# Kernel tuning notes

Measured on AMD Instinct MI355X. Metric: run time of the kernel, lower is better.

The kernel has to match this reference:

```python
import jax, jax.numpy as jnp
import numpy as np

N = 100_000          # nodes
E = 3_200_000        # edges (avg degree 32)
IN, HID, OUT = 128, 64, 40
POWERS = [6, 8, 10]
MAXP = 10
LN_EPS = 1e-5


def setup_inputs() -> dict:
    key = jax.random.key(0)
    ks = jax.random.split(key, 8)
    x = jax.random.normal(ks[0], (N, IN), jnp.float32)
    edge_index = jax.random.randint(ks[1], (2, E), 0, N, dtype=jnp.int32)
    # params (torch Linear: y = x @ W + b with W stored [in, out] here)
    W1 = jax.random.normal(ks[2], (IN, HID), jnp.float32) / np.sqrt(IN)
    b1 = jnp.zeros((HID,), jnp.float32)
    # MixHopConv has Linear for every power 0..max(powers); only p in POWERS are used
    Wc = jax.random.normal(ks[3], (MAXP + 1, HID, HID), jnp.float32) / np.sqrt(HID)
    bc = jnp.zeros((MAXP + 1, HID), jnp.float32)
    W2 = jax.random.normal(ks[4], (HID * len(POWERS), OUT), jnp.float32) / np.sqrt(HID * len(POWERS))
    b2 = jnp.zeros((OUT,), jnp.float32)
    g1 = jnp.ones((HID,), jnp.float32); be1 = jnp.zeros((HID,), jnp.float32)
    g2 = jnp.ones((HID * len(POWERS),), jnp.float32); be2 = jnp.zeros((HID * len(POWERS),), jnp.float32)
    return dict(x=x, edge_index=edge_index, W1=W1, b1=b1, Wc=Wc, bc=bc,
                W2=W2, b2=b2, g1=g1, be1=be1, g2=g2, be2=be2)


def _layer_norm(h, g, b):
    mu = jnp.mean(h, axis=-1, keepdims=True)
    var = jnp.mean(jnp.square(h - mu), axis=-1, keepdims=True)
    return (h - mu) * jax.lax.rsqrt(var + LN_EPS) * g + b


def _gcn_norm(edge_index, n, dtype):
    # add self loops (fill 1), symmetric normalization D^-1/2 (A+I) D^-1/2
    loops = jnp.arange(n, dtype=edge_index.dtype)
    src = jnp.concatenate([edge_index[0], loops])
    dst = jnp.concatenate([edge_index[1], loops])
    w = jnp.ones(src.shape[0], dtype)
    deg = jax.ops.segment_sum(w, dst, num_segments=n)
    dis = jnp.where(deg > 0, jax.lax.rsqrt(deg), 0.0)
    norm = dis[src] * w * dis[dst]
    return src, dst, norm


def reference(x, edge_index, W1, b1, Wc, bc, W2, b2, g1, be1, g2, be2):
    n = x.shape[0]
    src, dst, norm = _gcn_norm(edge_index, n, x.dtype)

    def propagate(h):  # out[i] = sum_{(j->i)} norm_ij * h[j]
        return jax.ops.segment_sum(norm[:, None] * h[src], dst, num_segments=n)

    h = jax.nn.gelu(x @ W1 + b1, approximate=False)
    h = _layer_norm(h, g1, be1)
    # dropout is identity in eval mode

    # MixHop: propagate MAXP times, apply per-power linear at p in POWERS
    outs = {}
    if 0 in POWERS:
        outs[0] = h @ Wc[0] + bc[0]
    cur = h
    for j in range(1, MAXP + 1):
        cur = propagate(cur)
        if j in POWERS:
            outs[j] = cur @ Wc[j] + bc[j]
    h = jnp.concatenate([outs[p] for p in POWERS], axis=-1)

    h = jax.nn.gelu(h, approximate=False)
    h = _layer_norm(h, g2, be2)
    return h @ W2 + b2
```

## Files before the change

### kernel.cpp

```cpp
#include <hip/hip_runtime.h>

typedef _Float16 h16;
typedef _Float16 h16x8 __attribute__((ext_vector_type(8)));
typedef short short8 __attribute__((ext_vector_type(8)));
typedef float f32x4 __attribute__((ext_vector_type(4)));

__device__ __forceinline__ float bf2f(unsigned short u) {
    return __uint_as_float(((unsigned)u) << 16);
}
__device__ __forceinline__ unsigned short f2bf(float f) {
    unsigned x = __float_as_uint(f);
    unsigned r = x + 0x7fffu + ((x >> 16) & 1u);
    return (unsigned short)(r >> 16);
}
__device__ __forceinline__ float gelu_fast(float v) {
    float y = 0.7978845608f * (v + 0.044715f * v * v * v);
    float e = __expf(2.0f * y);
    float th = 1.0f - 2.0f * __builtin_amdgcn_rcpf(e + 1.0f);
    return 0.5f * v * (1.0f + th);
}

__device__ __forceinline__ float ldin(const void* p, size_t i, int isbf) {
    return isbf ? bf2f(((const unsigned short*)p)[i]) : ((const float*)p)[i];
}

#define LN_EPS 1e-5f
#define NBMAX 256
#define NBLK 1024

__global__ void k_prep(const void* __restrict__ W1, const void* __restrict__ b1,
                       const void* __restrict__ g1, const void* __restrict__ be1,
                       const void* __restrict__ Wc, const void* __restrict__ bc,
                       const void* __restrict__ W2, const void* __restrict__ b2,
                       const void* __restrict__ g2, const void* __restrict__ be2,
                       int* __restrict__ flag,
                       short* __restrict__ W1f, h16* __restrict__ Wcf,
                       h16* __restrict__ W2f, float* __restrict__ vecs,
                       float2* __restrict__ GBv) {
    int isbf = (((const unsigned*)g1)[0] == 0x3F803F80u) ? 1 : 0;
    int t = threadIdx.x, b = blockIdx.x;
    if (b == 0) {
        for (int idx = t; idx < 1024; idx += 256) {
            int c = idx >> 8, tt = (idx >> 6) & 3, ln = idx & 63;
            int quad = ln >> 4, col = tt * 16 + (ln & 15);
#pragma unroll
            for (int j = 0; j < 8; j++) {
                int k = c * 32 + quad * 8 + j;
                W1f[idx * 8 + j] = (short)f2bf(ldin(W1, (size_t)k * 64 + col, isbf));
            }
        }
    } else if (b <= 3) {
        int s = b - 1;
        int js = (s == 0) ? 6 : (s == 1) ? 8 : 10;
        size_t woff = (size_t)js * 64 * 64;
        h16* Wp = Wcf + (size_t)s * 4096;
        for (int idx = t; idx < 512; idx += 256) {
            int c = idx >> 8, tt = (idx >> 6) & 3, ln = idx & 63;
            int quad = ln >> 4, col = tt * 16 + (ln & 15);
#pragma unroll
            for (int j = 0; j < 8; j++) {
                int k = c * 32 + quad * 8 + j;
                Wp[idx * 8 + j] = (h16)ldin(Wc, woff + (size_t)k * 64 + col, isbf);
            }
        }
    } else if (b == 4) {
        for (int idx = t; idx < 1152; idx += 256) {
            int c = idx / 192, rem = idx % 192;
            int tt = rem >> 6, ln = rem & 63;
            int quad = ln >> 4, col = tt * 16 + (ln & 15);
#pragma unroll
            for (int j = 0; j < 8; j++) {
                int k = c * 32 + quad * 8 + j;
                float w = (col < 40) ? ldin(W2, (size_t)k * 40 + col, isbf) : 0.0f;
                W2f[idx * 8 + j] = (h16)w;
            }
        }
    } else {
        if (t == 0) *flag = isbf;
        if (t < 64) {
            vecs[t]       = ldin(b1, t, isbf);
            vecs[64 + t]  = ldin(g1, t, isbf);
            vecs[128 + t] = ldin(be1, t, isbf);
            vecs[192 + t] = ldin(bc, (size_t)6 * 64 + t, isbf);
            vecs[256 + t] = ldin(bc, (size_t)8 * 64 + t, isbf);
            vecs[320 + t] = ldin(bc, (size_t)10 * 64 + t, isbf);
        }
        if (t < 40) vecs[384 + t] = ldin(b2, t, isbf);
        if (t < 192) {
            float2 gb; gb.x = ldin(g2, t, isbf); gb.y = ldin(be2, t, isbf);
            GBv[t] = gb;
        }
    }
}

__global__ void k_bcnt(const int* __restrict__ dst, int* __restrict__ bcnt,
                       int* __restrict__ cnts, int E, int chunk) {
    __shared__ int c[NBMAX];
    int t = threadIdx.x, blk = blockIdx.x;
    c[t] = 0;
    __syncthreads();
    int beg = blk * chunk;
    int end = beg + chunk; if (end > E) end = E;
    for (int i0 = beg + t * 4; i0 < end; i0 += 1024) {
        if (i0 + 4 <= end) {
            int4 d4 = *(const int4*)(dst + i0);
            atomicAdd(&c[d4.x >> 9], 1);
            atomicAdd(&c[d4.y >> 9], 1);
            atomicAdd(&c[d4.z >> 9], 1);
            atomicAdd(&c[d4.w >> 9], 1);
        } else {
            for (int i = i0; i < end; i++) atomicAdd(&c[dst[i] >> 9], 1);
        }
    }
    __syncthreads();
    cnts[blk * NBMAX + t] = c[t];
    if (c[t] > 0) atomicAdd(&bcnt[t], c[t]);
}

__global__ void k_colscan(const int* __restrict__ bcnt, const int* __restrict__ cnts,
                          int* __restrict__ bbase, int* __restrict__ base, int NB) {
    __shared__ int bsc[256];
    __shared__ int sh[256];
    __shared__ int bbs;
    int b = blockIdx.x, t = threadIdx.x;
    int bv = bcnt[t];
    bsc[t] = bv;
    __syncthreads();
    for (int s = 1; s < 256; s <<= 1) {
        int u = 0;
        if (t >= s) u = bsc[t - s];
        __syncthreads();
        bsc[t] += u;
        __syncthreads();
    }
    if (t == b) { bbs = bsc[t] - bv; bbase[b] = bbs; }
    if (b == 0 && t == 255) bbase[NB] = bsc[255];
    __syncthreads();
    int bb = bbs;
    int v[NBLK / 256];
    int s = 0;
#pragma unroll
    for (int j = 0; j < NBLK / 256; j++) {
        v[j] = cnts[(size_t)(t * (NBLK / 256) + j) * NBMAX + b];
        s += v[j];
    }
    sh[t] = s;
    __syncthreads();
    for (int st = 1; st < 256; st <<= 1) {
        int u = 0;
        if (t >= st) u = sh[t - st];
        __syncthreads();
        sh[t] += u;
        __syncthreads();
    }
    int run = bb + (t == 0 ? 0 : sh[t - 1]);
#pragma unroll
    for (int j = 0; j < NBLK / 256; j++) {
        base[(size_t)(t * (NBLK / 256) + j) * NBMAX + b] = run;
        run += v[j];
    }
}

__global__ void k_bin(const int* __restrict__ src, const int* __restrict__ dst,
                      const int* __restrict__ base, unsigned* __restrict__ stg,
                      int E, int chunk) {
    __shared__ int loc[NBMAX];
    int t = threadIdx.x, blk = blockIdx.x;
    loc[t] = base[(size_t)blk * NBMAX + t];
    __syncthreads();
    int beg = blk * chunk;
    int end = beg + chunk; if (end > E) end = E;
    for (int i0 = beg + t * 4; i0 < end; i0 += 1024) {
        bool full = (i0 + 4 <= end);
        int4 s4, d4;
        if (full) {
            s4 = *(const int4*)(src + i0);
            d4 = *(const int4*)(dst + i0);
        }
#pragma unroll
        for (int r = 0; r < 4; r++) {
            int i = i0 + r;
            int s, d;
            if (full) {
                s = ((const int*)&s4)[r]; d = ((const int*)&d4)[r];
            } else {
                if (i >= end) continue;
                s = src[i]; d = dst[i];
            }
            int b = d >> 9;
            unsigned pr = ((unsigned)(d & 511) << 23) | (unsigned)s;
            int p = atomicAdd(&loc[b], 1);
            stg[p] = pr;
        }
    }
}

__global__ void k_build2(const unsigned* __restrict__ stg, const int* __restrict__ bbase,
                         int* __restrict__ offv, float* __restrict__ dis,
                         float* __restrict__ d2, float* __restrict__ idis,
                         int* __restrict__ csr, int N, int E, int NB) {
    __shared__ int cnt2[4096];
    __shared__ int sc2[4096];
    __shared__ int pos2[4096];
    __shared__ int part[256];
    int b = blockIdx.x, t = threadIdx.x;
    for (int i = t; i < 4096; i += 256) { cnt2[i] = 0; pos2[i] = 0; }
    __syncthreads();
    int beg = bbase[b], end = bbase[b + 1];
    for (int k = beg + t; k < end; k += 256) {
        unsigned pr = stg[k];
        int dl = (int)(pr >> 23);
        int src = (int)(pr & 0x7FFFFFu);
        atomicAdd(&cnt2[dl * 8 + (src >> 14)], 1);
    }
    __syncthreads();
    int base16 = t * 16;
    int run = 0;
#pragma unroll
    for (int j = 0; j < 16; j++) { run += cnt2[base16 + j]; sc2[base16 + j] = run; }
    part[t] = run;
    __syncthreads();
    for (int s = 1; s < 256; s <<= 1) {
        int u = 0;
        if (t >= s) u = part[t - s];
        __syncthreads();
        part[t] += u;
        __syncthreads();
    }
    int add = (t == 0) ? 0 : part[t - 1];
#pragma unroll
    for (int j = 0; j < 16; j++) sc2[base16 + j] += add;
    __syncthreads();
    int nb9 = b << 9;
#pragma unroll
    for (int ii = 0; ii < 2; ii++) {
        int dl = t + ii * 256;
        int node = nb9 + dl;
        if (node < N) {
            int k0 = dl * 8;
            int startk = sc2[k0] - cnt2[k0];
            int deg = sc2[k0 + 7] - startk;
            offv[node] = beg + startk;
            float dp1 = (float)(deg + 1);
            dis[node] = rsqrtf(dp1);
            d2[node] = 1.0f / dp1;
            idis[node] = sqrtf(dp1);
        }
    }
    if (b == NB - 1 && t == 0) offv[N] = E;
    __syncthreads();
    for (int k = beg + t; k < end; k += 256) {
        unsigned pr = stg[k];
        int dl = (int)(pr >> 23);
        int src = (int)(pr & 0x7FFFFFu);
        int key = dl * 8 + (src >> 14);
        int p = beg + (sc2[key] - cnt2[key]) + atomicAdd(&pos2[key], 1);
        csr[p] = src;
    }
}

__global__ void k_in(const void* __restrict__ x, const short* __restrict__ W1f,
                     const float* __restrict__ vecs, const float* __restrict__ dis,
                     h16* __restrict__ h, const int* __restrict__ flag, int N) {
    __shared__ __align__(16) short Bf[4][4][64][8];
    int isbf = *flag;
    int tid = threadIdx.x;
    {
        int4* d = (int4*)&Bf[0][0][0][0];
        const int4* s4 = (const int4*)W1f;
        for (int i = tid; i < 1024; i += 256) d[i] = s4[i];
    }
    __syncthreads();
    int lane = tid & 63, quad = lane >> 4, m15 = lane & 15;
    float bcol[4], gcol[4], ecol[4];
#pragma unroll
    for (int t = 0; t < 4; t++) {
        int col = t * 16 + m15;
        bcol[t] = vecs[col];
        gcol[t] = vecs[64 + col];
        ecol[t] = vecs[128 + col];
    }
    int wave = blockIdx.x * 4 + (tid >> 6);
    int nwave = gridDim.x * 4;
    int ntile = (N + 15) >> 4;
    for (int tile = wave; tile < ntile; tile += nwave) {
        int m0 = tile << 4;
        int mrow = m0 + m15; if (mrow >= N) mrow = N - 1;
        f32x4 acc[4];
#pragma unroll
        for (int t = 0; t < 4; t++)
#pragma unroll
            for (int r = 0; r < 4; r++) acc[t][r] = 0.0f;
#pragma unroll
        for (int c = 0; c < 4; c++) {
            short8 a;
            if (isbf) {
                a = *(const short8*)((const unsigned short*)x + (size_t)mrow * 128 + c * 32 + quad * 8);
            } else {
                const float* xp = (const float*)x + (size_t)mrow * 128 + c * 32 + quad * 8;
#pragma unroll
                for (int j = 0; j < 8; j++) a[j] = (short)f2bf(xp[j]);
            }
#pragma unroll
            for (int t = 0; t < 4; t++) {
                short8 b = *(const short8*)(&Bf[c][t][lane][0]);
                acc[t] = __builtin_amdgcn_mfma_f32_16x16x32_bf16(a, b, acc[t], 0, 0, 0);
            }
        }
        float v[4][4];
        float s[4] = {0, 0, 0, 0}, q[4] = {0, 0, 0, 0};
#pragma unroll
        for (int t = 0; t < 4; t++)
#pragma unroll
            for (int r = 0; r < 4; r++) {
                float g = gelu_fast(acc[t][r] + bcol[t]);
                v[t][r] = g;
                s[r] += g; q[r] += g * g;
            }
#pragma unroll
        for (int o = 1; o < 16; o <<= 1)
#pragma unroll
            for (int r = 0; r < 4; r++) {
                s[r] += __shfl_xor(s[r], o, 64);
                q[r] += __shfl_xor(q[r], o, 64);
            }
#pragma unroll
        for (int r = 0; r < 4; r++) {
            int node = m0 + quad * 4 + r;
            if (node < N) {
                float mu = s[r] * (1.0f / 64.0f);
                float var = q[r] * (1.0f / 64.0f) - mu * mu;
                float rs = rsqrtf(var + LN_EPS);
                float dn = dis[node];
#pragma unroll
                for (int t = 0; t < 4; t++) {
                    float hv = (v[t][r] - mu) * rs * gcol[t] + ecol[t];
                    h[(size_t)node * 64 + t * 16 + m15] = (h16)(dn * hv);
                }
            }
        }
    }
}

__global__ void k_prop(const h16* __restrict__ cur, h16* __restrict__ nxt,
                       const int* __restrict__ offv, const int* __restrict__ csr,
                       const float* __restrict__ d2, int N) {
    int node = blockIdx.x * 4 + (threadIdx.x >> 6);
    if (node >= N) return;
    int lane = threadIdx.x & 63;
    int g = lane >> 2, q = lane & 3;
    h16x8 acc0 = {0, 0, 0, 0, 0, 0, 0, 0};
    h16x8 acc1 = {0, 0, 0, 0, 0, 0, 0, 0};
    int e = offv[node], end = offv[node + 1];
#pragma unroll 2
    for (; e + 16 <= end; e += 16) {
        int s = csr[e + g];
        const h16* rp = cur + (size_t)s * 64 + q * 16;
        acc0 += *(const h16x8*)(rp);
        acc1 += *(const h16x8*)(rp + 8);
    }
    int r = end - e;
    if (g < r) {
        int s = csr[e + g];
        const h16* rp = cur + (size_t)s * 64 + q * 16;
        acc0 += *(const h16x8*)(rp);
        acc1 += *(const h16x8*)(rp + 8);
    }
#pragma unroll
    for (int o = 4; o < 64; o <<= 1) {
        h16x8 o0, o1;
        int* a0 = (int*)&acc0; int* p0 = (int*)&o0;
        int* a1 = (int*)&acc1; int* p1 = (int*)&o1;
#pragma unroll
        for (int i = 0; i < 4; i++) {
            p0[i] = __shfl_xor(a0[i], o, 64);
            p1[i] = __shfl_xor(a1[i], o, 64);
        }
        acc0 += o0; acc1 += o1;
    }
    if (g == 0) {
        float dd = d2[node];
        const h16* sp = cur + (size_t)node * 64 + q * 16;
        h16x8 sv0 = *(const h16x8*)(sp);
        h16x8 sv1 = *(const h16x8*)(sp + 8);
        h16x8 o80, o81;
#pragma unroll
        for (int i = 0; i < 8; i++) {
            o80[i] = (h16)(dd * ((float)acc0[i] + (float)sv0[i]));
            o81[i] = (h16)(dd * ((float)acc1[i] + (float)sv1[i]));
        }
        h16* np = nxt + (size_t)node * 64 + q * 16;
        *(h16x8*)(np) = o80;
        *(h16x8*)(np + 8) = o81;
    }
}

__global__ void k_pout(const h16* __restrict__ cur, const h16* __restrict__ Wcf,
                       const float* __restrict__ bcv, const float* __restrict__ idis,
                       h16* __restrict__ hcat, int seg, int N) {
    __shared__ __align__(16) h16 Bf[2][4][64][8];
    int tid = threadIdx.x;
    {
        int4* d = (int4*)&Bf[0][0][0][0];
        const int4* s4 = (const int4*)Wcf;
        for (int i = tid; i < 512; i += 256) d[i] = s4[i];
    }
    __syncthreads();
    int lane = tid & 63, quad = lane >> 4, m15 = lane & 15;
    float bcol[4];
#pragma unroll
    for (int t = 0; t < 4; t++) bcol[t] = bcv[t * 16 + m15];
    int wave = blockIdx.x * 4 + (tid >> 6);
    int nwave = gridDim.x * 4;
    int ntile = (N + 15) >> 4;
    for (int tile = wave; tile < ntile; tile += nwave) {
        int m0 = tile << 4;
        int mrow = m0 + m15; if (mrow >= N) mrow = N - 1;
        f32x4 acc[4];
#pragma unroll
        for (int t = 0; t < 4; t++)
#pragma unroll
            for (int r = 0; r < 4; r++) acc[t][r] = 0.0f;
#pragma unroll
        for (int c = 0; c < 2; c++) {
            h16x8 a = *(const h16x8*)(cur + (size_t)mrow * 64 + c * 32 + quad * 8);
#pragma unroll
            for (int t = 0; t < 4; t++) {
                h16x8 b = *(const h16x8*)(&Bf[c][t][lane][0]);
                acc[t] = __builtin_amdgcn_mfma_f32_16x16x32_f16(a, b, acc[t], 0, 0, 0);
            }
        }
#pragma unroll
        for (int r = 0; r < 4; r++) {
            int node = m0 + quad * 4 + r;
            if (node < N) {
                float di = idis[node];
#pragma unroll
                for (int t = 0; t < 4; t++)
                    hcat[(size_t)node * 192 + seg * 64 + t * 16 + m15] =
                        (h16)(bcol[t] + di * acc[t][r]);
            }
        }
    }
}

__global__ void k_fin(const h16* __restrict__ hcat, const h16* __restrict__ W2f,
                      const float* __restrict__ b2v, const float2* __restrict__ GBv,
                      void* __restrict__ out, const int* __restrict__ flag, int N) {
    __shared__ __align__(16) h16 Bf[6][3][64][8];
    __shared__ float2 GBs[192];
    __shared__ __align__(16) h16 Y[4][16][200];
    int isbf = *flag;
    int tid = threadIdx.x;
    {
        int4* d = (int4*)&Bf[0][0][0][0];
        const int4* s4 = (const int4*)W2f;
        for (int i = tid; i < 1152; i += 256) d[i] = s4[i];
    }
    for (int i = tid; i < 192; i += 256) GBs[i] = GBv[i];
    __syncthreads();
    int wv = tid >> 6;
    int lane = tid & 63, quad = lane >> 4, m15 = lane & 15;
    float b2c[3];
#pragma unroll
    for (int t = 0; t < 3; t++) {
        int col = t * 16 + m15;
        b2c[t] = (col < 40) ? b2v[col] : 0.0f;
    }
    int wave = blockIdx.x * 4 + wv;
    int nwave = gridDim.x * 4;
    int ntile = (N + 15) >> 4;
    for (int tile = wave; tile < ntile; tile += nwave) {
        int m0 = tile << 4;
        int mrow = m0 + m15; if (mrow >= N) mrow = N - 1;
        const h16* hp = hcat + (size_t)mrow * 192 + quad * 48;
        float s = 0.0f, q = 0.0f;
#pragma unroll
        for (int u = 0; u < 6; u++) {
            h16x8 vv = *(const h16x8*)(hp + u * 8);
            h16x8 gv;
#pragma unroll
            for (int j = 0; j < 8; j++) {
                float g = gelu_fast((float)vv[j]);
                gv[j] = (h16)g;
                s += g; q += g * g;
            }
            *(h16x8*)(&Y[wv][m15][quad * 48 + u * 8]) = gv;
        }
        s += __shfl_xor(s, 16, 64); s += __shfl_xor(s, 32, 64);
        q += __shfl_xor(q, 16, 64); q += __shfl_xor(q, 32, 64);
        float mu = s * (1.0f / 192.0f);
        float var = q * (1.0f / 192.0f) - mu * mu;
        float rs = rsqrtf(var + LN_EPS);
        asm volatile("s_waitcnt lgkmcnt(0)" ::: "memory");
        f32x4 acc[3];
#pragma unroll
        for (int t = 0; t < 3; t++)
#pragma unroll
            for (int r = 0; r < 4; r++) acc[t][r] = 0.0f;
#pragma unroll
        for (int c = 0; c < 6; c++) {
            h16x8 raw = *(const h16x8*)(&Y[wv][m15][c * 32 + quad * 8]);
            h16x8 a;
#pragma unroll
            for (int j = 0; j < 8; j++) {
                int k = c * 32 + quad * 8 + j;
                float2 gb = GBs[k];
                a[j] = (h16)(((float)raw[j] - mu) * rs * gb.x + gb.y);
            }
#pragma unroll
            for (int t = 0; t < 3; t++) {
                h16x8 b = *(const h16x8*)(&Bf[c][t][lane][0]);
                acc[t] = __builtin_amdgcn_mfma_f32_16x16x32_f16(a, b, acc[t], 0, 0, 0);
            }
        }
        asm volatile("" ::: "memory");
#pragma unroll
        for (int r = 0; r < 4; r++) {
            int node = m0 + quad * 4 + r;
            if (node < N) {
#pragma unroll
                for (int t = 0; t < 3; t++) {
                    int col = t * 16 + m15;
                    if (col < 40) {
                        float o = acc[t][r] + b2c[t];
                        if (isbf) ((unsigned short*)out)[(size_t)node * 40 + col] = f2bf(o);
                        else      ((float*)out)[(size_t)node * 40 + col] = o;
                    }
                }
            }
        }
    }
}

extern "C" void kernel_launch(void* const* d_in, const int* in_sizes, int n_in,
                              void* d_out, int out_size, void* d_ws, size_t ws_size,
                              hipStream_t stream) {
    const int IN = 128, HID = 64;
    const int N = in_sizes[0] / IN;
    const int E = in_sizes[1] / 2;
    const int NB = (N + 511) >> 9;
    const int chunk = (((E + NBLK - 1) / NBLK) + 3) & ~3;

    const void* x   = d_in[0];
    const int*  ei  = (const int*)d_in[1];
    const void* W1  = d_in[2];
    const void* b1  = d_in[3];
    const void* Wc  = d_in[4];
    const void* bc  = d_in[5];
    const void* W2  = d_in[6];
    const void* b2  = d_in[7];
    const void* g1  = d_in[8];
    const void* be1 = d_in[9];
    const void* g2  = d_in[10];
    const void* be2 = d_in[11];

    char* ws = (char*)d_ws;
    size_t off = 0;
    auto take = [&](size_t bytes) -> char* {
        char* p = ws + off;
        off = (off + bytes + 255) & ~(size_t)255;
        return p;
    };
    int*   flag  = (int*)take(256);
    int*   bcnt  = (int*)take(NBMAX * 4);
    int*   bbase = (int*)take((NBMAX + 1) * 4);
    float* dis   = (float*)take((size_t)N * 4);
    float* d2    = (float*)take((size_t)N * 4);
    float* idis  = (float*)take((size_t)N * 4);
    int*   offv  = (int*)take((size_t)(N + 1) * 4);
    int*   csr   = (int*)take((size_t)E * 4);
    size_t unionSz = (size_t)E * 4 > (size_t)N * 384 ? (size_t)E * 4 : (size_t)N * 384;
    char*  uni   = take(unionSz);
    unsigned* stg = (unsigned*)uni;
    h16*   hcat  = (h16*)uni;
    h16*   hA    = (h16*)take((size_t)N * HID * 2);
    h16*   hB    = (h16*)take((size_t)N * HID * 2);
    short* W1f  = (short*)take(16384);
    h16*   Wcf  = (h16*)take(24576);
    h16*   W2f  = (h16*)take(18432);
    float* vecs = (float*)take(2048);
    float2* GBv = (float2*)take(1536);
    int*   cnts  = csr;
    int*   base  = csr + (size_t)NBLK * NBMAX;

    hipMemsetAsync(bcnt, 0, NBMAX * 4, stream);

    const int* srcp = ei;
    const int* dstp = ei + E;
    int gNode = (N + 3) / 4;
    int gDense = 1563;

    k_prep<<<6, 256, 0, stream>>>(W1, b1, g1, be1, Wc, bc, W2, b2, g2, be2, flag,
                                  W1f, Wcf, W2f, vecs, GBv);
    k_bcnt<<<NBLK, 256, 0, stream>>>(dstp, bcnt, cnts, E, chunk);
    k_colscan<<<NB, 256, 0, stream>>>(bcnt, cnts, bbase, base, NB);
    k_bin<<<NBLK, 256, 0, stream>>>(srcp, dstp, base, stg, E, chunk);
    k_build2<<<NB, 256, 0, stream>>>(stg, bbase, offv, dis, d2, idis, csr, N, E, NB);

    k_in<<<gDense, 256, 0, stream>>>(x, W1f, vecs, dis, hA, flag, N);
    h16* cur = hA; h16* nxt = hB;
    int seg = 0;
    for (int j = 1; j <= 10; j++) {
        k_prop<<<gNode, 256, 0, stream>>>(cur, nxt, offv, csr, d2, N);
        h16* tmp = cur; cur = nxt; nxt = tmp;
        if (j == 6 || j == 8 || j == 10) {
            k_pout<<<gDense, 256, 0, stream>>>(cur, Wcf + (size_t)seg * 4096,
                                               vecs + 192 + seg * 64, idis,
                                               hcat, seg, N);
            seg++;
        }
    }
    k_fin<<<gDense, 256, 0, stream>>>(hcat, W2f, vecs + 384, GBv, d_out, flag, N);
}
```

Baseline: 826.9 us.

## Sort edges locally in shared memory before binning; widen build and prop blocks

Adds a k_bin_sort kernel that counts and prefix-scans destination buckets per chunk in shared memory. Edges are placed bucket-contiguous in LDS, then copied out so global writes to the staging array come in runs instead of scattered atomics. k_build2 moves to 512 threads with one node per thread and 8-entry scan segments. k_prop moves to 512-thread blocks covering 8 nodes each. The new shared-memory sort only runs when the chunk fits CHCAP and adds a second pass over dst.

```diff
diff --git a/kernel.cpp b/kernel.cpp
--- a/kernel.cpp
+++ b/kernel.cpp
@@ -27,6 +27,7 @@
 #define LN_EPS 1e-5f
 #define NBMAX 256
 #define NBLK 1024
+#define CHCAP 3328
 
 __global__ void k_prep(const void* __restrict__ W1, const void* __restrict__ b1,
                        const void* __restrict__ g1, const void* __restrict__ be1,
@@ -161,6 +162,75 @@
     }
 }
 
+__global__ void k_bin_sort(const int* __restrict__ src, const int* __restrict__ dst,
+                           const int* __restrict__ base, unsigned* __restrict__ stg,
+                           int E, int chunk) {
+    __shared__ unsigned srt[CHCAP];
+    __shared__ unsigned char bbk[CHCAP];
+    __shared__ int cnt[NBMAX], lst[NBMAX], lpos[NBMAX], gbase[NBMAX];
+    __shared__ int sh[256];
+    int t = threadIdx.x, blk = blockIdx.x;
+    cnt[t] = 0; lpos[t] = 0;
+    gbase[t] = base[(size_t)blk * NBMAX + t];
+    __syncthreads();
+    int beg = blk * chunk;
+    int end = beg + chunk; if (end > E) end = E;
+    int cend = end - beg;
+    for (int i0 = beg + t * 4; i0 < end; i0 += 1024) {
+        if (i0 + 4 <= end) {
+            int4 d4 = *(const int4*)(dst + i0);
+            atomicAdd(&cnt[d4.x >> 9], 1);
+            atomicAdd(&cnt[d4.y >> 9], 1);
+            atomicAdd(&cnt[d4.z >> 9], 1);
+            atomicAdd(&cnt[d4.w >> 9], 1);
+        } else {
+            for (int i = i0; i < end; i++) atomicAdd(&cnt[dst[i] >> 9], 1);
+        }
+    }
+    __syncthreads();
+    int v = cnt[t];
+    sh[t] = v;
+    __syncthreads();
+    for (int s = 1; s < 256; s <<= 1) {
+        int u = 0;
+        if (t >= s) u = sh[t - s];
+        __syncthreads();
+        sh[t] += u;
+        __syncthreads();
+    }
+    lst[t] = sh[t] - v;
+    __syncthreads();
+    for (int i0 = beg + t * 4; i0 < end; i0 += 1024) {
+        bool full = (i0 + 4 <= end);
+        int4 s4, d4;
+        if (full) {
+            s4 = *(const int4*)(src + i0);
+            d4 = *(const int4*)(dst + i0);
+        }
+#pragma unroll
+        for (int r = 0; r < 4; r++) {
+            int i = i0 + r;
+            int s, d;
+            if (full) {
+                s = ((const int*)&s4)[r]; d = ((const int*)&d4)[r];
+            } else {
+                if (i >= end) continue;
+                s = src[i]; d = dst[i];
+            }
+            int b = d >> 9;
+            unsigned pr = ((unsigned)(d & 511) << 23) | (unsigned)s;
+            int p = lst[b] + atomicAdd(&lpos[b], 1);
+            srt[p] = pr;
+            bbk[p] = (unsigned char)b;
+        }
+    }
+    __syncthreads();
+    for (int i = t; i < cend; i += 256) {
+        int b = bbk[i];
+        stg[gbase[b] + (i - lst[b])] = srt[i];
+    }
+}
+
 __global__ void k_bin(const int* __restrict__ src, const int* __restrict__ dst,
                       const int* __restrict__ base, unsigned* __restrict__ stg,
                       int E, int chunk) {
@@ -202,25 +272,25 @@
     __shared__ int cnt2[4096];
     __shared__ int sc2[4096];
     __shared__ int pos2[4096];
-    __shared__ int part[256];
+    __shared__ int part[512];
     int b = blockIdx.x, t = threadIdx.x;
-    for (int i = t; i < 4096; i += 256) { cnt2[i] = 0; pos2[i] = 0; }
+    for (int i = t; i < 4096; i += 512) { cnt2[i] = 0; pos2[i] = 0; }
     __syncthreads();
     int beg = bbase[b], end = bbase[b + 1];
-    for (int k = beg + t; k < end; k += 256) {
+    for (int k = beg + t; k < end; k += 512) {
         unsigned pr = stg[k];
         int dl = (int)(pr >> 23);
         int src = (int)(pr & 0x7FFFFFu);
         atomicAdd(&cnt2[dl * 8 + (src >> 14)], 1);
     }
     __syncthreads();
-    int base16 = t * 16;
+    int base8 = t * 8;
     int run = 0;
 #pragma unroll
-    for (int j = 0; j < 16; j++) { run += cnt2[base16 + j]; sc2[base16 + j] = run; }
+    for (int j = 0; j < 8; j++) { run += cnt2[base8 + j]; sc2[base8 + j] = run; }
     part[t] = run;
     __syncthreads();
-    for (int s = 1; s < 256; s <<= 1) {
+    for (int s = 1; s < 512; s <<= 1) {
         int u = 0;
         if (t >= s) u = part[t - s];
         __syncthreads();
@@ -229,12 +299,11 @@
     }
     int add = (t == 0) ? 0 : part[t - 1];
 #pragma unroll
-    for (int j = 0; j < 16; j++) sc2[base16 + j] += add;
+    for (int j = 0; j < 8; j++) sc2[base8 + j] += add;
     __syncthreads();
     int nb9 = b << 9;
-#pragma unroll
-    for (int ii = 0; ii < 2; ii++) {
-        int dl = t + ii * 256;
+    {
+        int dl = t;
         int node = nb9 + dl;
         if (node < N) {
             int k0 = dl * 8;
@@ -249,7 +318,7 @@
     }
     if (b == NB - 1 && t == 0) offv[N] = E;
     __syncthreads();
-    for (int k = beg + t; k < end; k += 256) {
+    for (int k = beg + t; k < end; k += 512) {
         unsigned pr = stg[k];
         int dl = (int)(pr >> 23);
         int src = (int)(pr & 0x7FFFFFu);
@@ -345,7 +414,7 @@
 __global__ void k_prop(const h16* __restrict__ cur, h16* __restrict__ nxt,
                        const int* __restrict__ offv, const int* __restrict__ csr,
                        const float* __restrict__ d2, int N) {
-    int node = blockIdx.x * 4 + (threadIdx.x >> 6);
+    int node = blockIdx.x * 8 + (threadIdx.x >> 6);
     if (node >= N) return;
     int lane = threadIdx.x & 63;
     int g = lane >> 2, q = lane & 3;
@@ -588,21 +657,24 @@
 
     const int* srcp = ei;
     const int* dstp = ei + E;
-    int gNode = (N + 3) / 4;
+    int gNode = (N + 7) / 8;
     int gDense = 1563;
 
     k_prep<<<6, 256, 0, stream>>>(W1, b1, g1, be1, Wc, bc, W2, b2, g2, be2, flag,
                                   W1f, Wcf, W2f, vecs, GBv);
     k_bcnt<<<NBLK, 256, 0, stream>>>(dstp, bcnt, cnts, E, chunk);
     k_colscan<<<NB, 256, 0, stream>>>(bcnt, cnts, bbase, base, NB);
-    k_bin<<<NBLK, 256, 0, stream>>>(srcp, dstp, base, stg, E, chunk);
-    k_build2<<<NB, 256, 0, stream>>>(stg, bbase, offv, dis, d2, idis, csr, N, E, NB);
+    if (chunk <= CHCAP)
+        k_bin_sort<<<NBLK, 256, 0, stream>>>(srcp, dstp, base, stg, E, chunk);
+    else
+        k_bin<<<NBLK, 256, 0, stream>>>(srcp, dstp, base, stg, E, chunk);
+    k_build2<<<NB, 512, 0, stream>>>(stg, bbase, offv, dis, d2, idis, csr, N, E, NB);
 
     k_in<<<gDense, 256, 0, stream>>>(x, W1f, vecs, dis, hA, flag, N);
     h16* cur = hA; h16* nxt = hB;
     int seg = 0;
     for (int j = 1; j <= 10; j++) {
-        k_prop<<<gNode, 256, 0, stream>>>(cur, nxt, offv, csr, d2, N);
+        k_prop<<<gNode, 512, 0, stream>>>(cur, nxt, offv, csr, d2, N);
         h16* tmp = cur; cur = nxt; nxt = tmp;
         if (j == 6 || j == 8 || j == 10) {
             k_pout<<<gDense, 256, 0, stream>>>(cur, Wcf + (size_t)seg * 4096,
```

New measurement: 822.3 us. About the same (-0.6%).
